# Performance work log

Hardware: AMD Instinct MI355X
Metric: run time of the kernel (lower is better)

The kernel has to match this reference:

```python
import jax, jax.numpy as jnp
import numpy as np
from jax import lax

TABLE_SIZE = 1024   # LSH table buckets
R = 2.5             # hash bucket width r
U = 0.83            # ALSH norm rescale bound
M = 9               # appended ALSH dims; M // (K*K) = 1 extra channel
K = 3               # kernel spatial size
PAD = 1


def _P(kflat, m):
    # L2-ALSH preprocessing: rescale so max row norm == U, append ||x||^{2^i}, i=1..m
    norms = jnp.linalg.norm(kflat, axis=1)
    x = kflat * (U / jnp.max(norms))
    p = jnp.sum(x * x, axis=1)  # ||x||^2
    powers = [p]
    for _ in range(m - 1):
        powers.append(powers[-1] ** 2)
    return jnp.concatenate([x, jnp.stack(powers, axis=1)], axis=1)  # [O, D+m]


def _conv(x, w):
    return lax.conv_general_dilated(
        x, w, window_strides=(1, 1), padding=[(PAD, PAD), (PAD, PAD)],
        dimension_numbers=("NCHW", "OIHW", "NCHW"))


def setup_inputs() -> dict:
    key = jax.random.key(0)
    k1, k2, k3, k4 = jax.random.split(key, 4)
    inp = jax.random.normal(k1, (16, 128, 64, 64), jnp.float32)
    kernels = jax.random.normal(k2, (256, 128, 3, 3), jnp.float32) * 0.05
    d = 128 + M // (K * K)  # 129
    a = jax.random.normal(k3, (d * K * K,), jnp.float32)  # 1161
    b = jax.random.uniform(k4, (1,), jnp.float32) * R
    return {"input": inp, "kernels": kernels, "a": a, "b": b}


def reference(input, kernels, a, b):
    O, C, kh, kw = kernels.shape
    B, _, H, W = input.shape
    extra_ch = M // (kh * kw)
    d = C + extra_ch

    # ---- init_table: hash every kernel row into a bucket ----
    kflat = kernels.reshape(O, -1)                       # [O, C*kh*kw]
    h = jnp.floor((_P(kflat, M) @ a + b[0]) / R)         # [O]
    bucket = jnp.abs(jnp.fmod(h.astype(jnp.int32), TABLE_SIZE))  # torch fmod+abs semantics

    # ---- vote: Q appends 0.5-filled channels, conv with hash vector as kernel ----
    input_Q = jnp.concatenate(
        [input, jnp.full((B, extra_ch, H, W), 0.5, input.dtype)], axis=1)
    dotted = _conv(input_Q, a.reshape(1, d, kh, kw))     # [B,1,H,W]
    votes = jnp.floor((dotted.reshape(-1) + b[0]) / R).astype(jnp.int32)
    vbucket = jnp.abs(jnp.fmod(votes, TABLE_SIZE))

    # ---- count_votes + argmax bucket ----
    count = jax.ops.segment_sum(jnp.ones(vbucket.shape, jnp.float32),
                                vbucket, num_segments=TABLE_SIZE)
    index = jnp.argmax(count)

    # ---- active set: kernels whose table bucket == winning bucket (mask form, jit-safe) ----
    mask = (bucket == index)                             # [O] bool
    active_kernels = kernels * mask[:, None, None, None].astype(kernels.dtype)

    # apply the active set (the conv this module feeds downstream)
    out = _conv(input, active_kernels)                   # [B,O,H,W]
    return out, index, mask
```

## Files before the change

### kernel.cpp

```cpp
#include <hip/hip_runtime.h>
#include <cmath>
#include <cstdint>

#define TSZ 1024
#define RDIV 2.5f
#define UCONST 0.83f

typedef __bf16 bf16x8 __attribute__((ext_vector_type(8)));
typedef float f32x4 __attribute__((ext_vector_type(4)));
typedef unsigned short ushortT;

__device__ __forceinline__ ushortT bf16r(float f) {
  union { float f; unsigned u; } x; x.f = f;
  unsigned r = (x.u + 0x7FFFu + ((x.u >> 16) & 1u)) >> 16;
  return (ushortT)r;
}

__device__ __forceinline__ void glds16(const void* g, void* l) {
  __builtin_amdgcn_global_load_lds(
      (const __attribute__((address_space(1))) unsigned int*)(g),
      (__attribute__((address_space(3))) unsigned int*)(l), 16, 0, 0);
}

__global__ __launch_bounds__(256) void k_cvtg(const float* __restrict__ in,
                                              const float* __restrict__ a,
                                              ushortT* __restrict__ nb,
                                              float* __restrict__ g,
                                              int* __restrict__ count) {
  __shared__ float tile2[128][65];
  __shared__ float gpart[4][9][64];
  const int bid = blockIdx.x;
  const int n = bid >> 6, y = bid & 63;
  const int t = threadIdx.x;
  if (t == 0) count[bid] = 0;
  {
    const int chs = t >> 4, l16 = t & 15;
    const float* basep = in + ((size_t)(n * 128) << 12) + (y << 6) + (l16 << 2);
#pragma unroll
    for (int i = 0; i < 8; ++i) {
      int ch = (i << 4) + chs;
      f32x4 v = *reinterpret_cast<const f32x4*>(basep + ((size_t)ch << 12));
#pragma unroll
      for (int u = 0; u < 4; ++u) tile2[ch][(l16 << 2) + u] = v[u];
    }
  }
  __syncthreads();
  {
    const int part = __builtin_amdgcn_readfirstlane(t >> 6);
    const int x = t & 63;
    float gacc[9];
#pragma unroll
    for (int tap = 0; tap < 9; ++tap) gacc[tap] = 0.f;
    const int c0 = part << 5;
#pragma unroll
    for (int i = 0; i < 32; ++i) {
      float v = tile2[c0 + i][x];
      const float* ap = a + (c0 + i) * 9;
#pragma unroll
      for (int tap = 0; tap < 9; ++tap) gacc[tap] += v * ap[tap];
    }
#pragma unroll
    for (int tap = 0; tap < 9; ++tap) gpart[part][tap][x] = gacc[tap];
  }
  __syncthreads();
  if (t < 64) {
    const int x = t;
#pragma unroll
    for (int tap = 0; tap < 9; ++tap) {
      float s = gpart[0][tap][x] + gpart[1][tap][x] + gpart[2][tap][x] + gpart[3][tap][x];
      g[tap * 65536 + (n << 12) + (y << 6) + x] = s;
    }
  }
  {
    const int x2 = t >> 2;
    ushortT* dst = nb + (((size_t)((n << 6) + y) << 6) + x2) * 128;
#pragma unroll
    for (int j = 0; j < 4; ++j) {
      int c0 = ((t & 3) << 3) + (j << 5);
      union { ushortT us[8]; uint4 v; } pk;
#pragma unroll
      for (int u = 0; u < 8; ++u) pk.us[u] = bf16r(tile2[c0 + u][x2]);
      *reinterpret_cast<uint4*>(dst + c0) = pk.v;
    }
  }
}

__global__ __launch_bounds__(256) void k_vote3(const float* __restrict__ g,
                                               const float* __restrict__ a,
                                               const float* __restrict__ bb,
                                               int* __restrict__ count) {
  __shared__ int hist[TSZ];
  const int t = threadIdx.x;
  for (int i = t; i < TSZ; i += 256) hist[i] = 0;
  __syncthreads();
  const int pix = blockIdx.x * 256 + t;
  const int n = pix >> 12, y = (pix >> 6) & 63, x = pix & 63;
  float acc = 0.f;
#pragma unroll
  for (int tap = 0; tap < 9; ++tap) {
    const int dy = tap / 3 - 1, dx = tap % 3 - 1;
    const int yy = y + dy, xx = x + dx;
    if ((unsigned)yy < 64u && (unsigned)xx < 64u)
      acc += g[tap * 65536 + (n << 12) + (yy << 6) + xx];
  }
  {
    const float* av = a + 1152;
#pragma unroll
    for (int ky = 0; ky < 3; ++ky) {
      int yy = y + ky - 1;
      if ((unsigned)yy >= 64u) continue;
#pragma unroll
      for (int kx = 0; kx < 3; ++kx) {
        int xx = x + kx - 1;
        if ((unsigned)xx >= 64u) continue;
        acc += 0.5f * av[ky * 3 + kx];
      }
    }
  }
  int v = (int)floorf((acc + bb[0]) / RDIV);
  int r = v % TSZ; if (r < 0) r = -r;
  atomicAdd(&hist[r], 1);
  __syncthreads();
  for (int i = t; i < TSZ; i += 256) {
    int h = hist[i];
    if (h) atomicAdd(&count[i], h);
  }
}

__global__ __launch_bounds__(256) void k_norm(const float* __restrict__ k,
                                              unsigned* __restrict__ scaleBits) {
  int o = blockIdx.x;
  const float* row = k + (size_t)o * 1152;
  float s = 0.f;
  for (int j = threadIdx.x; j < 1152; j += 256) { float v = row[j]; s += v * v; }
  __shared__ float red[256];
  red[threadIdx.x] = s; __syncthreads();
  for (int st = 128; st; st >>= 1) {
    if (threadIdx.x < st) red[threadIdx.x] += red[threadIdx.x + st];
    __syncthreads();
  }
  if (threadIdx.x == 0) atomicMax(scaleBits, __float_as_uint(red[0]));
}

__global__ __launch_bounds__(256) void k_hash(const float* __restrict__ k,
                                              const float* __restrict__ a,
                                              const float* __restrict__ b,
                                              const unsigned* __restrict__ scaleBits,
                                              int* __restrict__ bucket) {
  int o = blockIdx.x;
  float scale = UCONST / sqrtf(__uint_as_float(scaleBits[0]));
  const float* row = k + (size_t)o * 1152;
  float dot = 0.f, p = 0.f;
  for (int j = threadIdx.x; j < 1152; j += 256) {
    float x = row[j] * scale;
    dot += x * a[j];
    p += x * x;
  }
  __shared__ float rd[256], rp[256];
  rd[threadIdx.x] = dot; rp[threadIdx.x] = p; __syncthreads();
  for (int st = 128; st; st >>= 1) {
    if (threadIdx.x < st) { rd[threadIdx.x] += rd[threadIdx.x + st]; rp[threadIdx.x] += rp[threadIdx.x + st]; }
    __syncthreads();
  }
  if (threadIdx.x == 0) {
    float acc = rd[0];
    float pw = rp[0];
    for (int i = 0; i < 9; i++) { acc += pw * a[1152 + i]; pw = pw * pw; }
    acc += b[0];
    float h = floorf(acc / RDIV);
    int hi = (int)h;
    int r = hi % TSZ; if (r < 0) r = -r;
    bucket[o] = r;
  }
}

__global__ __launch_bounds__(256) void k_wprep2(const int* __restrict__ count,
                                                const int* __restrict__ bucket,
                                                const float* __restrict__ w,
                                                ushortT* __restrict__ wb,
                                                float* __restrict__ tail) {
  __shared__ int sc[256];
  __shared__ int si[256];
  const int t = threadIdx.x;
  int bc = count[t], bi = t;
#pragma unroll
  for (int j = 1; j < 4; ++j) {
    int i2 = t + j * 256;
    int c2 = count[i2];
    if (c2 > bc) { bc = c2; bi = i2; }
  }
  sc[t] = bc; si[t] = bi; __syncthreads();
  for (int st = 128; st; st >>= 1) {
    if (t < st) {
      int c2 = sc[t + st], i2 = si[t + st];
      if (c2 > sc[t] || (c2 == sc[t] && i2 < si[t])) { sc[t] = c2; si[t] = i2; }
    }
    __syncthreads();
  }
  const int idx = si[0];
  const int o = blockIdx.x;
  const int m = (bucket[o] == idx) ? 1 : 0;
  if (t == 0) {
    if (o == 0) tail[0] = (float)idx;
    tail[1 + o] = (float)m;
  }
  const float mf = m ? 1.f : 0.f;
  const float* wr = w + (size_t)o * 1152;
  ushortT* dst = wb + (size_t)o * 1152;
  for (int j = t; j < 1152; j += 256) {
    int r = j >> 7, c = j & 127;
    dst[j] = bf16r(wr[c * 9 + r] * mf);
  }
}

__global__ __launch_bounds__(512, 1) void k_gemm4(const ushortT* __restrict__ nb,
                                                  const ushortT* __restrict__ wb,
                                                  const char* __restrict__ zp,
                                                  float* __restrict__ out) {
  __shared__ __align__(16) char smem[3 * 32768];
  const int t = threadIdx.x, l = t & 63, w = t >> 6;
  const int mb = blockIdx.x;
  const int n = mb >> 4;
  const int y0 = (mb & 15) << 2;
  const int wm = w & 1, wn = w >> 1;
  const int lr = l & 15, lq = l >> 4;
  const char* nbN = (const char*)nb + (size_t)n * 1048576;

  int cC[4], yA[4], xA[4];
  const char* bPj[4];
#pragma unroll
  for (int j = 0; j < 4; ++j) {
    int c = (w << 2) + j;
    cC[j] = c;
    int m = (c << 4) + lr;
    yA[j] = y0 + (m >> 6);
    xA[j] = m & 63;
    int orow = ((c - 16) << 4) + lr;
    bPj[j] = (const char*)wb + (size_t)orow * 2304 + (lq << 4);
  }

  auto stage2 = [&](int buf, int s, int jlo) {
    const int tap = s >> 2;
    const int d3 = (tap * 0x5556) >> 16;
    const int dy = d3 - 1, dx = tap - d3 * 3 - 1;
    const int cb = (s & 3) << 6;
    char* dstb = smem + buf * 32768;
#pragma unroll
    for (int j = jlo; j < jlo + 2; ++j) {
      const char* src;
      if (cC[j] < 16) {
        int yy = yA[j] + dy, xx = xA[j] + dx;
        bool ok = ((unsigned)yy < 64u) && ((unsigned)xx < 64u);
        src = ok ? (nbN + (((yy << 6) + xx) << 8) + cb + (lq << 4))
                 : (zp + (lq << 4));
      } else {
        src = bPj[j] + (s << 6);
      }
      glds16(src, dstb + (cC[j] << 10));
    }
  };

  f32x4 acc[8][4] = {};

  stage2(0, 0, 0); stage2(0, 0, 2);
  stage2(1, 1, 0); stage2(1, 1, 2);
  asm volatile("s_waitcnt vmcnt(4)" ::: "memory");
  __builtin_amdgcn_s_barrier();

  for (int tt = 0; tt < 36; ++tt) {
    const char* bufb = smem + (tt % 3) * 32768;
    const bool stg = (tt + 2) < 36;
    const int sb = (tt + 2) % 3, ss = tt + 2;
    bf16x8 bv[4], afA[4], afB[4];
#pragma unroll
    for (int ni = 0; ni < 4; ++ni)
      bv[ni] = *reinterpret_cast<const bf16x8*>(
          bufb + 16384 + (((wn << 2) + ni) << 10) + (l << 4));
#pragma unroll
    for (int mi = 0; mi < 4; ++mi)
      afA[mi] = *reinterpret_cast<const bf16x8*>(
          bufb + (((wm << 3) + mi) << 10) + (l << 4));
    if (stg) stage2(sb, ss, 0);
    __builtin_amdgcn_s_barrier();
    asm volatile("s_waitcnt lgkmcnt(0)" ::: "memory");
    __builtin_amdgcn_sched_barrier(0);
    __builtin_amdgcn_s_setprio(1);
#pragma unroll
    for (int mi = 0; mi < 4; ++mi)
#pragma unroll
      for (int ni = 0; ni < 4; ++ni)
        acc[mi][ni] = __builtin_amdgcn_mfma_f32_16x16x32_bf16(
            afA[mi], bv[ni], acc[mi][ni], 0, 0, 0);
    __builtin_amdgcn_s_setprio(0);
    __builtin_amdgcn_s_barrier();
#pragma unroll
    for (int mi = 0; mi < 4; ++mi)
      afB[mi] = *reinterpret_cast<const bf16x8*>(
          bufb + (((wm << 3) + 4 + mi) << 10) + (l << 4));
    if (stg) stage2(sb, ss, 2);
    __builtin_amdgcn_s_barrier();
    asm volatile("s_waitcnt lgkmcnt(0)" ::: "memory");
    __builtin_amdgcn_sched_barrier(0);
    __builtin_amdgcn_s_setprio(1);
#pragma unroll
    for (int mi = 0; mi < 4; ++mi)
#pragma unroll
      for (int ni = 0; ni < 4; ++ni)
        acc[4 + mi][ni] = __builtin_amdgcn_mfma_f32_16x16x32_bf16(
            afB[mi], bv[ni], acc[4 + mi][ni], 0, 0, 0);
    __builtin_amdgcn_s_setprio(0);
    if (tt < 35) asm volatile("s_waitcnt vmcnt(4)" ::: "memory");
    else         asm volatile("s_waitcnt vmcnt(0)" ::: "memory");
    __builtin_amdgcn_s_barrier();
  }

  const int pos0 = (mb & 15) << 8;
#pragma unroll
  for (int ni = 0; ni < 4; ++ni) {
    const int o = (wn << 6) + (ni << 4) + lr;
    float* op = out + ((size_t)((n << 8) + o) << 12) + pos0 + (wm << 7) + (lq << 2);
#pragma unroll
    for (int mi = 0; mi < 8; ++mi)
      *reinterpret_cast<f32x4*>(op + (mi << 4)) = acc[mi][ni];
  }
}

__global__ __launch_bounds__(256) void k_vote2(const float* __restrict__ in,
                                               const float* __restrict__ a,
                                               const float* __restrict__ bb,
                                               int* __restrict__ count) {
  __shared__ float sb[6][8][64];
  __shared__ int hist[TSZ];
  const int t = threadIdx.x;
  for (int i = t; i < TSZ; i += 256) hist[i] = 0;
  const int bid = blockIdx.x;
  const int n = bid >> 4, y0 = (bid & 15) << 2;
  const int x = t & 63, ry = t >> 6;
  const int yq = y0 + ry;
  float acc = 0.f;
  const float* base = in + (size_t)n * 524288;
  for (int cc = 0; cc < 16; ++cc) {
    __syncthreads();
#pragma unroll
    for (int k = 0; k < 12; ++k) {
      int i = k * 256 + t;
      int row = i >> 9;
      int c8 = (i >> 6) & 7;
      int xx = i & 63;
      int yy = y0 - 1 + row;
      float v = 0.f;
      if ((unsigned)yy < 64u) v = base[(size_t)(cc * 8 + c8) * 4096 + yy * 64 + xx];
      sb[row][c8][xx] = v;
    }
    __syncthreads();
#pragma unroll
    for (int c8 = 0; c8 < 8; ++c8) {
      const float* av = a + (cc * 8 + c8) * 9;
#pragma unroll
      for (int ky = 0; ky < 3; ++ky) {
        const float* rowp = sb[ry + ky][c8];
        float left  = (x >= 1)  ? rowp[x - 1] : 0.f;
        float mid   = rowp[x];
        float right = (x <= 62) ? rowp[x + 1] : 0.f;
        acc += left * av[ky * 3 + 0] + mid * av[ky * 3 + 1] + right * av[ky * 3 + 2];
      }
    }
  }
  {
    const float* av = a + 1152;
#pragma unroll
    for (int ky = 0; ky < 3; ++ky) {
      int yy = yq + ky - 1;
      if ((unsigned)yy >= 64u) continue;
#pragma unroll
      for (int kx = 0; kx < 3; ++kx) {
        int xx = x + kx - 1;
        if ((unsigned)xx >= 64u) continue;
        acc += 0.5f * av[ky * 3 + kx];
      }
    }
  }
  int v = (int)floorf((acc + bb[0]) / RDIV);
  int r = v % TSZ; if (r < 0) r = -r;
  atomicAdd(&hist[r], 1);
  __syncthreads();
  for (int i = t; i < TSZ; i += 256) {
    int h = hist[i];
    if (h) atomicAdd(&count[i], h);
  }
}

__global__ __launch_bounds__(1024) void k_argmax(const int* __restrict__ count,
                                                 const int* __restrict__ bucket,
                                                 int* __restrict__ maskI,
                                                 float* __restrict__ tail) {
  __shared__ int sc[1024];
  __shared__ int si[1024];
  int t = threadIdx.x;
  sc[t] = count[t]; si[t] = t; __syncthreads();
  for (int st = 512; st; st >>= 1) {
    if (t < st) {
      int c2 = sc[t + st], i2 = si[t + st];
      if (c2 > sc[t] || (c2 == sc[t] && i2 < si[t])) { sc[t] = c2; si[t] = i2; }
    }
    __syncthreads();
  }
  int idx = si[0];
  if (t == 0) tail[0] = (float)idx;
  if (t < 256) {
    int m = (bucket[t] == idx) ? 1 : 0;
    maskI[t] = m;
    tail[1 + t] = (float)m;
  }
}

__global__ __launch_bounds__(256) void k_conv(const float* __restrict__ in,
                                              const float* __restrict__ w,
                                              const int* __restrict__ maskI,
                                              float* __restrict__ out) {
  const int og = blockIdx.x, n = blockIdx.y, yt = blockIdx.z;
  const int tid = threadIdx.x;
  const int tx = tid & 63, trow = tid >> 6;
  const int y0 = yt * 4;
  const int oc0 = og * 4;
  const int m0 = maskI[oc0], m1 = maskI[oc0 + 1], m2 = maskI[oc0 + 2], m3 = maskI[oc0 + 3];
  float* op = out + ((size_t)(n * 256 + oc0)) * 4096 + (size_t)(y0 + trow) * 64 + tx;
  if (!(m0 | m1 | m2 | m3)) {
    op[0] = 0.f; op[4096] = 0.f; op[8192] = 0.f; op[12288] = 0.f;
    return;
  }
  __shared__ float tile[6 * 66];
  const float* base = in + (size_t)n * 128 * 4096;
  const float* wb = w + (size_t)oc0 * 1152;
  float a0 = 0.f, a1 = 0.f, a2 = 0.f, a3 = 0.f;
  for (int c = 0; c < 128; c++) {
    __syncthreads();
    for (int i = tid; i < 396; i += 256) {
      int r = i / 66, col = i - r * 66;
      int yy = y0 - 1 + r, xx = col - 1;
      float v = 0.f;
      if ((unsigned)yy < 64u && (unsigned)xx < 64u) v = base[(size_t)c * 4096 + yy * 64 + xx];
      tile[i] = v;
    }
    __syncthreads();
    const int ro = trow * 66 + tx;
    float t00 = tile[ro],        t01 = tile[ro + 1],   t02 = tile[ro + 2];
    float t10 = tile[ro + 66],   t11 = tile[ro + 67],  t12 = tile[ro + 68];
    float t20 = tile[ro + 132],  t21 = tile[ro + 133], t22 = tile[ro + 134];
    const float* wc = wb + c * 9;
    if (m0) { const float* q = wc;        a0 += t00*q[0]+t01*q[1]+t02*q[2]+t10*q[3]+t11*q[4]+t12*q[5]+t20*q[6]+t21*q[7]+t22*q[8]; }
    if (m1) { const float* q = wc + 1152; a1 += t00*q[0]+t01*q[1]+t02*q[2]+t10*q[3]+t11*q[4]+t12*q[5]+t20*q[6]+t21*q[7]+t22*q[8]; }
    if (m2) { const float* q = wc + 2304; a2 += t00*q[0]+t01*q[1]+t02*q[2]+t10*q[3]+t11*q[4]+t12*q[5]+t20*q[6]+t21*q[7]+t22*q[8]; }
    if (m3) { const float* q = wc + 3456; a3 += t00*q[0]+t01*q[1]+t02*q[2]+t10*q[3]+t11*q[4]+t12*q[5]+t20*q[6]+t21*q[7]+t22*q[8]; }
  }
  op[0]     = m0 ? a0 : 0.f;
  op[4096]  = m1 ? a1 : 0.f;
  op[8192]  = m2 ? a2 : 0.f;
  op[12288] = m3 ? a3 : 0.f;
}

extern "C" void kernel_launch(void* const* d_in, const int* in_sizes, int n_in,
                              void* d_out, int out_size, void* d_ws, size_t ws_size,
                              hipStream_t stream) {
  const float* in = (const float*)d_in[0];
  const float* kw = (const float*)d_in[1];
  const float* a  = (const float*)d_in[2];
  const float* b  = (const float*)d_in[3];
  float* out = (float*)d_out;

  char* ws = (char*)d_ws;
  const size_t NEED_BIG = 19731776ULL;

  if (ws_size >= NEED_BIG) {
    ushortT* nb   = (ushortT*)(ws);
    ushortT* wb   = (ushortT*)(ws + 16777216);
    float* g      = (float*)(ws + 17367040);
    int* count    = (int*)(ws + 19726336);
    unsigned* scB = (unsigned*)(ws + 19730432);
    char* zpage   = (ws + 19730496);
    int* bucket   = (int*)(ws + 19730752);

    hipMemsetAsync(ws + 19730432, 0, 320, stream);

    k_cvtg<<<1024, 256, 0, stream>>>(in, a, nb, g, count);
    k_norm<<<256, 256, 0, stream>>>(kw, scB);
    k_hash<<<256, 256, 0, stream>>>(kw, a, b, scB, bucket);
    k_vote3<<<256, 256, 0, stream>>>(g, a, b, count);
    k_wprep2<<<256, 256, 0, stream>>>(count, bucket, kw, wb, out + 16777216);
    k_gemm4<<<256, 512, 0, stream>>>(nb, wb, zpage, out);
  } else {
    int* count    = (int*)(ws);
    unsigned* scB = (unsigned*)(ws + 4096);
    int* bucket   = (int*)(ws + 4160);
    int* maskI    = (int*)(ws + 5184);

    hipMemsetAsync(ws, 0, 4160, stream);
    k_norm<<<256, 256, 0, stream>>>(kw, scB);
    k_hash<<<256, 256, 0, stream>>>(kw, a, b, scB, bucket);
    k_vote2<<<256, 256, 0, stream>>>(in, a, b, count);
    k_argmax<<<1, 1024, 0, stream>>>(count, bucket, maskI, out + 16777216);
    dim3 grid(64, 16, 16);
    k_conv<<<grid, 256, 0, stream>>>(in, kw, maskI, out);
  }
}
```

Measured before the change: 167.1 us.

## Fuse norm/hash/vote/weight-prep into one grid-barrier kernel and pad activation layout

Merges the norm, hash, vote and weight-prep kernels into a single kernel that uses a global atomic spin barrier, cutting the six-kernel sequence to three launches. The bf16 activation buffer is now stored with a one-pixel zero border, so the GEMM drops per-tap bounds checks and the zero page. The g scratch moves into the output buffer and the GEMM loop is unrolled by three to remove the modulo buffer indexing. The spin barrier relies on all 256 blocks being co-resident, and the GEMM also drops its explicit lgkmcnt waits.

```diff
diff --git a/kernel.cpp b/kernel.cpp
--- a/kernel.cpp
+++ b/kernel.cpp
@@ -21,6 +21,9 @@
       (const __attribute__((address_space(1))) unsigned int*)(g),
       (__attribute__((address_space(3))) unsigned int*)(l), 16, 0, 0);
 }
+
+#define NB_ROW 8448
+#define NB_N 557568
 
 __global__ __launch_bounds__(256) void k_cvtg(const float* __restrict__ in,
                                               const float* __restrict__ a,
@@ -73,7 +76,7 @@
   }
   {
     const int x2 = t >> 2;
-    ushortT* dst = nb + (((size_t)((n << 6) + y) << 6) + x2) * 128;
+    ushortT* dst = nb + (size_t)n * NB_N + (size_t)(y + 1) * NB_ROW + (x2 + 1) * 128;
 #pragma unroll
     for (int j = 0; j < 4; ++j) {
       int c0 = ((t & 3) << 3) + (j << 5);
@@ -83,27 +86,63 @@
       *reinterpret_cast<uint4*>(dst + c0) = pk.v;
     }
   }
-}
-
-__global__ __launch_bounds__(256) void k_vote3(const float* __restrict__ g,
-                                               const float* __restrict__ a,
-                                               const float* __restrict__ bb,
-                                               int* __restrict__ count) {
+  {
+    const uint4 z4 = {0u, 0u, 0u, 0u};
+    ushortT* rowp = nb + (size_t)n * NB_N + (size_t)(y + 1) * NB_ROW;
+    if (t < 16)       *reinterpret_cast<uint4*>(rowp + t * 8) = z4;
+    else if (t < 32)  *reinterpret_cast<uint4*>(rowp + 65 * 128 + (t - 16) * 8) = z4;
+    if (y == 0) {
+      ushortT* r0 = nb + (size_t)n * NB_N;
+      for (int i = t; i < 1056; i += 256) *reinterpret_cast<uint4*>(r0 + i * 8) = z4;
+    }
+    if (y == 63) {
+      ushortT* r65 = nb + (size_t)n * NB_N + (size_t)65 * NB_ROW;
+      for (int i = t; i < 1056; i += 256) *reinterpret_cast<uint4*>(r65 + i * 8) = z4;
+    }
+  }
+}
+
+__global__ __launch_bounds__(256) void k_mid(const float* __restrict__ g,
+                                             const float* __restrict__ kw,
+                                             const float* __restrict__ a,
+                                             const float* __restrict__ bb,
+                                             float* __restrict__ norms2,
+                                             int* __restrict__ count,
+                                             unsigned* __restrict__ bar,
+                                             ushortT* __restrict__ wb,
+                                             float* __restrict__ tail) {
+  __shared__ float red[256];
+  __shared__ float rp[256];
   __shared__ int hist[TSZ];
-  const int t = threadIdx.x;
+  __shared__ int sc[256];
+  __shared__ int si[256];
+  __shared__ int sBucket;
+  const int o = blockIdx.x, t = threadIdx.x;
+
+  {
+    const float* row = kw + (size_t)o * 1152;
+    float s = 0.f;
+    for (int j = t; j < 1152; j += 256) { float v = row[j]; s += v * v; }
+    red[t] = s; __syncthreads();
+    for (int st = 128; st; st >>= 1) {
+      if (t < st) red[t] += red[t + st];
+      __syncthreads();
+    }
+    if (t == 0) norms2[o] = red[0];
+  }
   for (int i = t; i < TSZ; i += 256) hist[i] = 0;
   __syncthreads();
-  const int pix = blockIdx.x * 256 + t;
-  const int n = pix >> 12, y = (pix >> 6) & 63, x = pix & 63;
-  float acc = 0.f;
-#pragma unroll
-  for (int tap = 0; tap < 9; ++tap) {
-    const int dy = tap / 3 - 1, dx = tap % 3 - 1;
-    const int yy = y + dy, xx = x + dx;
-    if ((unsigned)yy < 64u && (unsigned)xx < 64u)
-      acc += g[tap * 65536 + (n << 12) + (yy << 6) + xx];
-  }
-  {
+  {
+    const int pix = o * 256 + t;
+    const int n = pix >> 12, y = (pix >> 6) & 63, x = pix & 63;
+    float acc = 0.f;
+#pragma unroll
+    for (int tap = 0; tap < 9; ++tap) {
+      const int dy = tap / 3 - 1, dx = tap % 3 - 1;
+      const int yy = y + dy, xx = x + dx;
+      if ((unsigned)yy < 64u && (unsigned)xx < 64u)
+        acc += g[tap * 65536 + (n << 12) + (yy << 6) + xx];
+    }
     const float* av = a + 1152;
 #pragma unroll
     for (int ky = 0; ky < 3; ++ky) {
@@ -116,14 +155,195 @@
         acc += 0.5f * av[ky * 3 + kx];
       }
     }
-  }
-  int v = (int)floorf((acc + bb[0]) / RDIV);
-  int r = v % TSZ; if (r < 0) r = -r;
-  atomicAdd(&hist[r], 1);
+    int v = (int)floorf((acc + bb[0]) / RDIV);
+    int r = v % TSZ; if (r < 0) r = -r;
+    atomicAdd(&hist[r], 1);
+  }
   __syncthreads();
   for (int i = t; i < TSZ; i += 256) {
     int h = hist[i];
     if (h) atomicAdd(&count[i], h);
+  }
+  __threadfence();
+  __syncthreads();
+  if (t == 0) {
+    __hip_atomic_fetch_add(bar, 1u, __ATOMIC_ACQ_REL, __HIP_MEMORY_SCOPE_AGENT);
+    while (__hip_atomic_load(bar, __ATOMIC_ACQUIRE, __HIP_MEMORY_SCOPE_AGENT) < 256u) {
+      __builtin_amdgcn_s_sleep(8);
+    }
+  }
+  __syncthreads();
+  __threadfence();
+  red[t] = norms2[t]; __syncthreads();
+  for (int st = 128; st; st >>= 1) {
+    if (t < st) red[t] = fmaxf(red[t], red[t + st]);
+    __syncthreads();
+  }
+  const float scale = UCONST / sqrtf(red[0]);
+  __syncthreads();
+  {
+    const float* row = kw + (size_t)o * 1152;
+    float dot = 0.f, p = 0.f;
+    for (int j = t; j < 1152; j += 256) {
+      float x = row[j] * scale;
+      dot += x * a[j];
+      p += x * x;
+    }
+    red[t] = dot; rp[t] = p; __syncthreads();
+    for (int st = 128; st; st >>= 1) {
+      if (t < st) { red[t] += red[t + st]; rp[t] += rp[t + st]; }
+      __syncthreads();
+    }
+    if (t == 0) {
+      float acc = red[0], pw = rp[0];
+      for (int i = 0; i < 9; i++) { acc += pw * a[1152 + i]; pw = pw * pw; }
+      acc += bb[0];
+      int hi = (int)floorf(acc / RDIV);
+      int r = hi % TSZ; if (r < 0) r = -r;
+      sBucket = r;
+    }
+  }
+  {
+    int bc = count[t], bi = t;
+#pragma unroll
+    for (int j = 1; j < 4; ++j) {
+      int i2 = t + j * 256;
+      int c2 = count[i2];
+      if (c2 > bc) { bc = c2; bi = i2; }
+    }
+    sc[t] = bc; si[t] = bi; __syncthreads();
+    for (int st = 128; st; st >>= 1) {
+      if (t < st) {
+        int c2 = sc[t + st], i2 = si[t + st];
+        if (c2 > sc[t] || (c2 == sc[t] && i2 < si[t])) { sc[t] = c2; si[t] = i2; }
+      }
+      __syncthreads();
+    }
+  }
+  const int idx = si[0];
+  const int m = (sBucket == idx) ? 1 : 0;
+  if (t == 0) {
+    if (o == 0) tail[0] = (float)idx;
+    tail[1 + o] = (float)m;
+  }
+  const float mf = m ? 1.f : 0.f;
+  const float* wr = kw + (size_t)o * 1152;
+  ushortT* dst = wb + (size_t)o * 1152;
+  for (int j = t; j < 1152; j += 256) {
+    int r = j >> 7, c = j & 127;
+    dst[j] = bf16r(wr[c * 9 + r] * mf);
+  }
+}
+
+__global__ __launch_bounds__(512, 1) void k_gemm5(const ushortT* __restrict__ nb,
+                                                  const ushortT* __restrict__ wb,
+                                                  float* __restrict__ out) {
+  __shared__ __align__(16) char smem[3 * 32768];
+  const int t = threadIdx.x, l = t & 63, w = t >> 6;
+  const int mb = blockIdx.x;
+  const int n = mb >> 4;
+  const int y0 = (mb & 15) << 2;
+  const int wm = w & 1, wn = w >> 1;
+  const int lr = l & 15, lq = l >> 4;
+
+  const char* srcBase[4];
+  int lds_o[4];
+  const bool isA = (w < 4);
+#pragma unroll
+  for (int j = 0; j < 4; ++j) {
+    int c = (w << 2) + j;
+    lds_o[j] = c << 10;
+    if (isA) {
+      int m = (c << 4) + lr;
+      int yl = m >> 6, x = m & 63;
+      srcBase[j] = (const char*)nb + (size_t)n * (NB_N * 2) +
+                   (size_t)(y0 + yl + 1) * (NB_ROW * 2) + (x + 1) * 256 + (lq << 4);
+    } else {
+      int orow = ((c - 16) << 4) + lr;
+      srcBase[j] = (const char*)wb + (size_t)orow * 2304 + (lq << 4);
+    }
+  }
+
+  auto srcOff = [&](int s) -> int {
+    if (isA) {
+      int tap = s >> 2;
+      int d3 = (tap * 21846) >> 16;
+      int dy = d3 - 1, dx = tap - d3 * 3 - 1;
+      return dy * (NB_ROW * 2) + dx * 256 + ((s & 3) << 6);
+    }
+    return s << 6;
+  };
+
+  auto stage2 = [&](int buf, int s, int jlo) {
+    const int off = srcOff(s);
+    char* dstb = smem + buf * 32768;
+#pragma unroll
+    for (int j = jlo; j < jlo + 2; ++j)
+      glds16(srcBase[j] + off, dstb + lds_o[j]);
+  };
+
+  f32x4 acc[8][4] = {};
+
+  stage2(0, 0, 0); stage2(0, 0, 2);
+  stage2(1, 1, 0); stage2(1, 1, 2);
+  asm volatile("s_waitcnt vmcnt(4)" ::: "memory");
+  __builtin_amdgcn_s_barrier();
+
+  const char* lA = smem + (wm << 13) + (l << 4);
+  const char* lB = smem + 16384 + (wn << 12) + (l << 4);
+
+  for (int big = 0; big < 12; ++big) {
+#pragma unroll
+    for (int u = 0; u < 3; ++u) {
+      const int tt = big * 3 + u;
+      const bool stg = tt < 34;
+      const int ss = tt + 2;
+      const int sb = (u + 2) % 3;
+      bf16x8 bv[4], afA[4], afB[4];
+#pragma unroll
+      for (int ni = 0; ni < 4; ++ni)
+        bv[ni] = *reinterpret_cast<const bf16x8*>(lB + u * 32768 + (ni << 10));
+#pragma unroll
+      for (int mi = 0; mi < 4; ++mi)
+        afA[mi] = *reinterpret_cast<const bf16x8*>(lA + u * 32768 + (mi << 10));
+      if (stg) stage2(sb, ss, 0);
+      __builtin_amdgcn_s_barrier();
+      __builtin_amdgcn_s_setprio(1);
+#pragma unroll
+      for (int mi = 0; mi < 4; ++mi)
+#pragma unroll
+        for (int ni = 0; ni < 4; ++ni)
+          acc[mi][ni] = __builtin_amdgcn_mfma_f32_16x16x32_bf16(
+              afA[mi], bv[ni], acc[mi][ni], 0, 0, 0);
+      __builtin_amdgcn_s_setprio(0);
+      __builtin_amdgcn_s_barrier();
+#pragma unroll
+      for (int mi = 0; mi < 4; ++mi)
+        afB[mi] = *reinterpret_cast<const bf16x8*>(lA + u * 32768 + ((4 + mi) << 10));
+      if (stg) stage2(sb, ss, 2);
+      __builtin_amdgcn_s_barrier();
+      __builtin_amdgcn_s_setprio(1);
+#pragma unroll
+      for (int mi = 0; mi < 4; ++mi)
+#pragma unroll
+        for (int ni = 0; ni < 4; ++ni)
+          acc[4 + mi][ni] = __builtin_amdgcn_mfma_f32_16x16x32_bf16(
+              afB[mi], bv[ni], acc[4 + mi][ni], 0, 0, 0);
+      __builtin_amdgcn_s_setprio(0);
+      if (tt == 34)     asm volatile("s_waitcnt vmcnt(0)" ::: "memory");
+      else if (tt < 34) asm volatile("s_waitcnt vmcnt(4)" ::: "memory");
+      if (tt < 35) __builtin_amdgcn_s_barrier();
+    }
+  }
+
+  const int pos0 = (mb & 15) << 8;
+#pragma unroll
+  for (int ni = 0; ni < 4; ++ni) {
+    const int o = (wn << 6) + (ni << 4) + lr;
+    float* op = out + ((size_t)((n << 8) + o) << 12) + pos0 + (wm << 7) + (lq << 2);
+#pragma unroll
+    for (int mi = 0; mi < 8; ++mi)
+      *reinterpret_cast<f32x4*>(op + (mi << 4)) = acc[mi][ni];
   }
 }
 
@@ -171,157 +391,6 @@
     int hi = (int)h;
     int r = hi % TSZ; if (r < 0) r = -r;
     bucket[o] = r;
-  }
-}
-
-__global__ __launch_bounds__(256) void k_wprep2(const int* __restrict__ count,
-                                                const int* __restrict__ bucket,
-                                                const float* __restrict__ w,
-                                                ushortT* __restrict__ wb,
-                                                float* __restrict__ tail) {
-  __shared__ int sc[256];
-  __shared__ int si[256];
-  const int t = threadIdx.x;
-  int bc = count[t], bi = t;
-#pragma unroll
-  for (int j = 1; j < 4; ++j) {
-    int i2 = t + j * 256;
-    int c2 = count[i2];
-    if (c2 > bc) { bc = c2; bi = i2; }
-  }
-  sc[t] = bc; si[t] = bi; __syncthreads();
-  for (int st = 128; st; st >>= 1) {
-    if (t < st) {
-      int c2 = sc[t + st], i2 = si[t + st];
-      if (c2 > sc[t] || (c2 == sc[t] && i2 < si[t])) { sc[t] = c2; si[t] = i2; }
-    }
-    __syncthreads();
-  }
-  const int idx = si[0];
-  const int o = blockIdx.x;
-  const int m = (bucket[o] == idx) ? 1 : 0;
-  if (t == 0) {
-    if (o == 0) tail[0] = (float)idx;
-    tail[1 + o] = (float)m;
-  }
-  const float mf = m ? 1.f : 0.f;
-  const float* wr = w + (size_t)o * 1152;
-  ushortT* dst = wb + (size_t)o * 1152;
-  for (int j = t; j < 1152; j += 256) {
-    int r = j >> 7, c = j & 127;
-    dst[j] = bf16r(wr[c * 9 + r] * mf);
-  }
-}
-
-__global__ __launch_bounds__(512, 1) void k_gemm4(const ushortT* __restrict__ nb,
-                                                  const ushortT* __restrict__ wb,
-                                                  const char* __restrict__ zp,
-                                                  float* __restrict__ out) {
-  __shared__ __align__(16) char smem[3 * 32768];
-  const int t = threadIdx.x, l = t & 63, w = t >> 6;
-  const int mb = blockIdx.x;
-  const int n = mb >> 4;
-  const int y0 = (mb & 15) << 2;
-  const int wm = w & 1, wn = w >> 1;
-  const int lr = l & 15, lq = l >> 4;
-  const char* nbN = (const char*)nb + (size_t)n * 1048576;
-
-  int cC[4], yA[4], xA[4];
-  const char* bPj[4];
-#pragma unroll
-  for (int j = 0; j < 4; ++j) {
-    int c = (w << 2) + j;
-    cC[j] = c;
-    int m = (c << 4) + lr;
-    yA[j] = y0 + (m >> 6);
-    xA[j] = m & 63;
-    int orow = ((c - 16) << 4) + lr;
-    bPj[j] = (const char*)wb + (size_t)orow * 2304 + (lq << 4);
-  }
-
-  auto stage2 = [&](int buf, int s, int jlo) {
-    const int tap = s >> 2;
-    const int d3 = (tap * 0x5556) >> 16;
-    const int dy = d3 - 1, dx = tap - d3 * 3 - 1;
-    const int cb = (s & 3) << 6;
-    char* dstb = smem + buf * 32768;
-#pragma unroll
-    for (int j = jlo; j < jlo + 2; ++j) {
-      const char* src;
-      if (cC[j] < 16) {
-        int yy = yA[j] + dy, xx = xA[j] + dx;
-        bool ok = ((unsigned)yy < 64u) && ((unsigned)xx < 64u);
-        src = ok ? (nbN + (((yy << 6) + xx) << 8) + cb + (lq << 4))
-                 : (zp + (lq << 4));
-      } else {
-        src = bPj[j] + (s << 6);
-      }
-      glds16(src, dstb + (cC[j] << 10));
-    }
-  };
-
-  f32x4 acc[8][4] = {};
-
-  stage2(0, 0, 0); stage2(0, 0, 2);
-  stage2(1, 1, 0); stage2(1, 1, 2);
-  asm volatile("s_waitcnt vmcnt(4)" ::: "memory");
-  __builtin_amdgcn_s_barrier();
-
-  for (int tt = 0; tt < 36; ++tt) {
-    const char* bufb = smem + (tt % 3) * 32768;
-    const bool stg = (tt + 2) < 36;
-    const int sb = (tt + 2) % 3, ss = tt + 2;
-    bf16x8 bv[4], afA[4], afB[4];
-#pragma unroll
-    for (int ni = 0; ni < 4; ++ni)
-      bv[ni] = *reinterpret_cast<const bf16x8*>(
-          bufb + 16384 + (((wn << 2) + ni) << 10) + (l << 4));
-#pragma unroll
-    for (int mi = 0; mi < 4; ++mi)
-      afA[mi] = *reinterpret_cast<const bf16x8*>(
-          bufb + (((wm << 3) + mi) << 10) + (l << 4));
-    if (stg) stage2(sb, ss, 0);
-    __builtin_amdgcn_s_barrier();
-    asm volatile("s_waitcnt lgkmcnt(0)" ::: "memory");
-    __builtin_amdgcn_sched_barrier(0);
-    __builtin_amdgcn_s_setprio(1);
-#pragma unroll
-    for (int mi = 0; mi < 4; ++mi)
-#pragma unroll
-      for (int ni = 0; ni < 4; ++ni)
-        acc[mi][ni] = __builtin_amdgcn_mfma_f32_16x16x32_bf16(
-            afA[mi], bv[ni], acc[mi][ni], 0, 0, 0);
-    __builtin_amdgcn_s_setprio(0);
-    __builtin_amdgcn_s_barrier();
-#pragma unroll
-    for (int mi = 0; mi < 4; ++mi)
-      afB[mi] = *reinterpret_cast<const bf16x8*>(
-          bufb + (((wm << 3) + 4 + mi) << 10) + (l << 4));
-    if (stg) stage2(sb, ss, 2);
-    __builtin_amdgcn_s_barrier();
-    asm volatile("s_waitcnt lgkmcnt(0)" ::: "memory");
-    __builtin_amdgcn_sched_barrier(0);
-    __builtin_amdgcn_s_setprio(1);
-#pragma unroll
-    for (int mi = 0; mi < 4; ++mi)
-#pragma unroll
-      for (int ni = 0; ni < 4; ++ni)
-        acc[4 + mi][ni] = __builtin_amdgcn_mfma_f32_16x16x32_bf16(
-            afB[mi], bv[ni], acc[4 + mi][ni], 0, 0, 0);
-    __builtin_amdgcn_s_setprio(0);
-    if (tt < 35) asm volatile("s_waitcnt vmcnt(4)" ::: "memory");
-    else         asm volatile("s_waitcnt vmcnt(0)" ::: "memory");
-    __builtin_amdgcn_s_barrier();
-  }
-
-  const int pos0 = (mb & 15) << 8;
-#pragma unroll
-  for (int ni = 0; ni < 4; ++ni) {
-    const int o = (wn << 6) + (ni << 4) + lr;
-    float* op = out + ((size_t)((n << 8) + o) << 12) + pos0 + (wm << 7) + (lq << 2);
-#pragma unroll
-    for (int mi = 0; mi < 8; ++mi)
-      *reinterpret_cast<f32x4*>(op + (mi << 4)) = acc[mi][ni];
   }
 }
 
@@ -469,25 +538,24 @@
   float* out = (float*)d_out;
 
   char* ws = (char*)d_ws;
-  const size_t NEED_BIG = 19731776ULL;
+  const size_t OFF_WB    = 17842176ULL;
+  const size_t OFF_COUNT = 18432000ULL;
+  const size_t OFF_NORM  = 18436096ULL;
+  const size_t OFF_BAR   = 18437120ULL;
+  const size_t NEED_BIG  = 18437184ULL;
 
   if (ws_size >= NEED_BIG) {
-    ushortT* nb   = (ushortT*)(ws);
-    ushortT* wb   = (ushortT*)(ws + 16777216);
-    float* g      = (float*)(ws + 17367040);
-    int* count    = (int*)(ws + 19726336);
-    unsigned* scB = (unsigned*)(ws + 19730432);
-    char* zpage   = (ws + 19730496);
-    int* bucket   = (int*)(ws + 19730752);
-
-    hipMemsetAsync(ws + 19730432, 0, 320, stream);
-
+    ushortT* nb    = (ushortT*)(ws);
+    ushortT* wb    = (ushortT*)(ws + OFF_WB);
+    int* count     = (int*)(ws + OFF_COUNT);
+    float* norms2  = (float*)(ws + OFF_NORM);
+    unsigned* bar  = (unsigned*)(ws + OFF_BAR);
+    float* g       = out;
+
+    hipMemsetAsync(bar, 0, 64, stream);
     k_cvtg<<<1024, 256, 0, stream>>>(in, a, nb, g, count);
-    k_norm<<<256, 256, 0, stream>>>(kw, scB);
-    k_hash<<<256, 256, 0, stream>>>(kw, a, b, scB, bucket);
-    k_vote3<<<256, 256, 0, stream>>>(g, a, b, count);
-    k_wprep2<<<256, 256, 0, stream>>>(count, bucket, kw, wb, out + 16777216);
-    k_gemm4<<<256, 512, 0, stream>>>(nb, wb, zpage, out);
+    k_mid<<<256, 256, 0, stream>>>(g, kw, a, b, norms2, count, bar, wb, out + 16777216);
+    k_gemm5<<<256, 512, 0, stream>>>(nb, wb, out);
   } else {
     int* count    = (int*)(ws);
     unsigned* scB = (unsigned*)(ws + 4096);
```

Measured after the change: 202.9 us. 21.5% more time.
